# Optimization experiments

Hardware: AMD Instinct MI355X
Metric: run time of the kernel (lower is better)

The kernel has to match this reference:

```python
import math
import jax, jax.numpy as jnp
import numpy as np

X_DIM = 512
Y_DIM = 512
DS = 4
WH, WW = Y_DIM // DS, X_DIM // DS
RADIUS = 6          # search_radius
PATCH = 21          # patch_size
SIGMA = 1.0         # preprocess_sigma
DELTA = 0.2
MASK_TH = 0.05
RAIN_TH = 0.1


def _blur(x, sigma=SIGMA):
    # replicate-pad + depthwise 2D gaussian conv (matches _gaussian_blur2d)
    r = max(1, int(math.ceil(3.0 * sigma)))
    c = jnp.arange(-r, r + 1, dtype=x.dtype)
    k1 = jnp.exp(-(c * c) / (2.0 * sigma * sigma))
    k1 = k1 / jnp.sum(k1)
    k2 = jnp.outer(k1, k1)
    C = x.shape[1]
    kern = jnp.broadcast_to(k2[None, None], (C, 1, 2 * r + 1, 2 * r + 1))
    xp = jnp.pad(x, ((0, 0), (0, 0), (r, r), (r, r)), mode='edge')
    return jax.lax.conv_general_dilated(xp, kern, (1, 1), 'VALID',
                                        dimension_numbers=('NCHW', 'OIHW', 'NCHW'),
                                        feature_group_count=C)


def _resize(x, oh, ow):
    # torch bilinear, align_corners=False, no antialias
    ih, iw = x.shape[-2], x.shape[-1]
    def coords(o, i):
        s = (jnp.arange(o, dtype=jnp.float32) + 0.5) * (i / o) - 0.5
        s = jnp.maximum(s, 0.0)
        i0 = jnp.minimum(jnp.floor(s).astype(jnp.int32), i - 1)
        i1 = jnp.minimum(i0 + 1, i - 1)
        return i0, i1, s - i0.astype(jnp.float32)
    y0, y1, wy = coords(oh, ih)
    x0, x1, wx = coords(ow, iw)
    r0 = x[..., y0, :]
    r1 = x[..., y1, :]
    v00 = r0[..., x0]; v01 = r0[..., x1]
    v10 = r1[..., x0]; v11 = r1[..., x1]
    wy = wy[:, None]; wx = wx[None, :]
    return v00 * (1 - wy) * (1 - wx) + v01 * (1 - wy) * wx + v10 * wy * (1 - wx) + v11 * wy * wx


def _avg_pool(x, k):
    # avg_pool2d, stride 1, padding k//2, count_include_pad=True
    p = k // 2
    nd = x.ndim
    win = (1,) * (nd - 2) + (k, k)
    pads = ((0, 0),) * (nd - 2) + ((p, p), (p, p))
    s = jax.lax.reduce_window(x, 0.0, jax.lax.add, win, (1,) * nd, pads)
    return s / float(k * k)


def _prepare(f):
    w = jnp.log1p(jnp.maximum(f, 0.0))
    w = _resize(w, WH, WW)
    return _blur(w)


def _grid_sample_border(field, grid):
    # bilinear grid_sample, padding_mode='border', align_corners=True
    B, C, H, W = field.shape
    ix = jnp.clip((grid[..., 0] + 1.0) * 0.5 * (W - 1), 0.0, W - 1)
    iy = jnp.clip((grid[..., 1] + 1.0) * 0.5 * (H - 1), 0.0, H - 1)
    x0 = jnp.floor(ix).astype(jnp.int32); y0 = jnp.floor(iy).astype(jnp.int32)
    x1 = jnp.minimum(x0 + 1, W - 1); y1 = jnp.minimum(y0 + 1, H - 1)
    wx = (ix - x0)[..., None]; wy = (iy - y0)[..., None]
    b = jnp.arange(B)[:, None, None]
    v00 = field[b, :, y0, x0]; v01 = field[b, :, y0, x1]
    v10 = field[b, :, y1, x0]; v11 = field[b, :, y1, x1]  # each [B,H,W,C]
    out = v00 * (1 - wy) * (1 - wx) + v01 * (1 - wy) * wx + v10 * wy * (1 - wx) + v11 * wy * wx
    return jnp.transpose(out, (0, 3, 1, 2))


def setup_inputs() -> dict:
    key = jax.random.key(0)
    k1, k2, k3 = jax.random.split(key, 3)
    pred = jax.random.normal(k1, (16, 1, 512, 512), dtype=jnp.float32)
    target = jax.random.uniform(k2, (16, 1, 512, 512), dtype=jnp.float32)
    ref = jax.random.uniform(k3, (16, 1, 512, 512), dtype=jnp.float32)
    return {"pred": pred, "target": target, "ref": ref}


def reference(pred, target, ref):
    prev_w = _prepare(ref)      # [B,1,WH,WW]
    curr_w = _prepare(target)
    rain = (_resize(target, WH, WW) >= RAIN_TH).astype(jnp.float32)
    n = 2 * RADIUS + 1
    offs = jnp.arange(-RADIUS, RADIUS + 1)
    dys = jnp.repeat(offs, n)   # dy outer loop
    dxs = jnp.tile(offs, n)     # dx inner loop
    rows = jnp.arange(WH); cols = jnp.arange(WW)

    def shift_cost(dy, dx):
        # replicate-border shift of curr_w by (dy,dx), then local SSD (21x21 avg)
        sh = curr_w[:, :, jnp.clip(rows + dy, 0, WH - 1), :]
        sh = sh[:, :, :, jnp.clip(cols + dx, 0, WW - 1)]
        return _avg_pool((prev_w - sh) ** 2, PATCH)

    costs = jax.vmap(shift_cost)(dys, dxs)        # [S,B,1,WH,WW]
    best = jnp.argmin(costs, axis=0)[:, 0]        # [B,WH,WW] (first-min, matches torch)
    fx = dxs.astype(jnp.float32)[best][:, None] * rain   # [B,1,WH,WW]
    fy = dys.astype(jnp.float32)[best][:, None] * rain
    fx = _blur(fx) * rain
    fy = _blur(fy) * rain
    fx = _resize(fx, Y_DIM, X_DIM) * (X_DIM / WW)
    fy = _resize(fy, Y_DIM, X_DIM) * (Y_DIM / WH)

    yy, xx = jnp.meshgrid(jnp.linspace(-1.0, 1.0, Y_DIM),
                          jnp.linspace(-1.0, 1.0, X_DIM), indexing='ij')
    gx = xx[None] - fx[:, 0] * (2.0 / (X_DIM - 1))
    gy = yy[None] - fy[:, 0] * (2.0 / (Y_DIM - 1))
    teacher = jnp.maximum(_grid_sample_border(ref, jnp.stack([gx, gy], axis=-1)), 0.0)

    d = pred - teacher
    ad = jnp.abs(d)
    loss = jnp.where(ad < DELTA, 0.5 * d * d, DELTA * (ad - 0.5 * DELTA))  # huber
    mask = ((teacher > MASK_TH) | (target > MASK_TH)).astype(loss.dtype)
    return jnp.mean(loss * mask)
```

## Files before the change

kernel.cpp:

```cpp
#include <hip/hip_runtime.h>
#include <math.h>

#define BATCH 16
#define HR 512
#define LR 128
#define N_LR (BATCH*LR*LR)
#define N_HR (BATCH*HR*HR)
#define NSH 13
#define NSHIFT 169
#define TH 8
#define NW 8

__device__ __forceinline__ int clampi(int v, int lo, int hi){ return v<lo?lo:(v>hi?hi:v); }

__device__ __forceinline__ float gk(int t){
  const float e1 = 0.60653065971263342f;
  const float e2 = 0.13533528323661270f;
  const float e3 = 0.011108996538242306f;
  const float norm = 1.0f/(1.0f + 2.0f*(e1+e2+e3));
  int a = t < 0 ? -t : t;
  float v = (a==0) ? 1.0f : (a==1 ? e1 : (a==2 ? e2 : e3));
  return v*norm;
}

__global__ void k_downsample(const float* __restrict__ ref, const float* __restrict__ tar,
                             float* __restrict__ wref, float* __restrict__ wtar,
                             float* __restrict__ rain){
  int i = blockIdx.x*blockDim.x + threadIdx.x;
  if (i >= N_LR) return;
  int x = i & (LR-1); int y = (i >> 7) & (LR-1); int b = i >> 14;
  int base = b*HR*HR + (4*y+1)*HR + 4*x;
  float4 r1 = *(const float4*)(ref + base);
  float4 r2 = *(const float4*)(ref + base + HR);
  float4 t1 = *(const float4*)(tar + base);
  float4 t2 = *(const float4*)(tar + base + HR);
  float r00=r1.y, r01=r1.z, r10=r2.y, r11=r2.z;
  float t00=t1.y, t01=t1.z, t10=t2.y, t11=t2.z;
  wref[i] = 0.25f*(log1pf(fmaxf(r00,0.f))+log1pf(fmaxf(r01,0.f))
                 +log1pf(fmaxf(r10,0.f))+log1pf(fmaxf(r11,0.f)));
  wtar[i] = 0.25f*(log1pf(fmaxf(t00,0.f))+log1pf(fmaxf(t01,0.f))
                 +log1pf(fmaxf(t10,0.f))+log1pf(fmaxf(t11,0.f)));
  rain[i] = (0.25f*(t00+t01+t10+t11) >= 0.1f) ? 1.0f : 0.0f;
}

__global__ void k_blur2(const float* __restrict__ in0, const float* __restrict__ in1,
                        float* __restrict__ out0, float* __restrict__ out1,
                        const float* __restrict__ m0, const float* __restrict__ m1){
  const int z = blockIdx.z;
  const float* in  = z ? in1 : in0;
  float* out       = z ? out1 : out0;
  const float* msk = z ? m1 : m0;
  const int r0 = blockIdx.x * 16;
  const int bb = blockIdx.y;
  const int tid = threadIdx.x;
  const float* I = in + (bb<<14);
  __shared__ float raw[22][LR];
  __shared__ float hb[22][LR];
  for (int idx = tid; idx < 22*LR; idx += 256){
    int lr = idx >> 7, c = idx & (LR-1);
    int gr = clampi(r0 - 3 + lr, 0, LR-1);
    raw[lr][c] = I[(gr<<7) + c];
  }
  __syncthreads();
  for (int idx = tid; idx < 22*LR; idx += 256){
    int lr = idx >> 7, c = idx & (LR-1);
    float s = 0.f;
    #pragma unroll
    for (int t=-3;t<=3;++t) s += gk(t)*raw[lr][clampi(c+t,0,LR-1)];
    hb[lr][c] = s;
  }
  __syncthreads();
  for (int idx = tid; idx < 16*LR; idx += 256){
    int lr = idx >> 7, c = idx & (LR-1);
    int i = r0 + lr;
    float s = 0.f;
    #pragma unroll
    for (int t=-3;t<=3;++t) s += gk(t)*hb[clampi(i+t,0,LR-1) - (r0-3)][c];
    int gi = (bb<<14) + (i<<7) + c;
    if (msk) s *= msk[gi];
    out[gi] = s;
  }
}

template<int CTRL, int RM>
__device__ __forceinline__ float dpp_mov0(float x){
  return __int_as_float(__builtin_amdgcn_update_dpp(0, __float_as_int(x), CTRL, RM, 0xF, true));
}
__device__ __forceinline__ float prefix64(float x){
  x += dpp_mov0<0x111,0xF>(x);
  x += dpp_mov0<0x112,0xF>(x);
  x += dpp_mov0<0x114,0xF>(x);
  x += dpp_mov0<0x118,0xF>(x);
  x += dpp_mov0<0x142,0xA>(x);
  x += dpp_mov0<0x143,0xC>(x);
  return x;
}
__device__ __forceinline__ float bperm(int addr4, float v){
  return __int_as_float(__builtin_amdgcn_ds_bpermute(addr4, __float_as_int(v)));
}

struct TapCtx { int ia0, ib0, ia1, ib1; bool la0hi, lb0ok, lb1hi, selA, selB; };

__device__ __forceinline__ void horiz_update(const TapCtx& tc, float v0, float v1, int s,
                                             unsigned long long& k0ref, unsigned long long& k1ref){
  float pf0 = prefix64(v0);
  float pf1 = prefix64(v1);
  float T0 = __int_as_float(__builtin_amdgcn_readlane(__float_as_int(pf0), 63));
  float va = tc.selA ? pf0 : pf1;
  float vb = tc.selB ? pf0 : pf1;
  float a0 = bperm(tc.ia0, va) + (tc.la0hi ? T0 : 0.f);
  float b0 = tc.lb0ok ? bperm(tc.ib0, pf0) : 0.f;
  float a1 = bperm(tc.ia1, pf1) + T0;
  float b1 = bperm(tc.ib1, vb) + (tc.lb1hi ? T0 : 0.f);
  float c0 = fmaxf((a0 - b0) * (1.0f/441.0f), 0.f);
  float c1 = fmaxf((a1 - b1) * (1.0f/441.0f), 0.f);
  unsigned long long k0 = ((unsigned long long)__float_as_uint(c0) << 32) | (unsigned)s;
  unsigned long long k1 = ((unsigned long long)__float_as_uint(c1) << 32) | (unsigned)s;
  if (k0 < k0ref) k0ref = k0;
  if (k1 < k1ref) k1ref = k1;
}

__global__ void __launch_bounds__(512, 2)
k_cost_flow(const float* __restrict__ prev, const float* __restrict__ curr,
            const float* __restrict__ rain,
            float* __restrict__ fx, float* __restrict__ fy){
  const int r0 = blockIdx.x * TH;
  const int bb = blockIdx.y;
  const int tid = threadIdx.x;
  const int w = tid >> 6, lane = tid & 63;
  const float* P = prev + (bb<<14);
  const float* C = curr + (bb<<14);

  __shared__ float currT[40][LR];
  __shared__ unsigned long long mg[4][TH*LR];

  for (int idx = tid; idx < 40*LR; idx += 512){
    int lr = idx >> 7, c = idx & (LR-1);
    int gr = clampi(r0 - 16 + lr, 0, LR-1);
    currT[lr][c] = C[(gr<<7) + c];
  }

  float p0[28], p1[28];
  #pragma unroll
  for (int wr = 0; wr < 28; ++wr){
    int gr = r0 - 10 + wr;
    if (gr >= 0 && gr < LR){ p0[wr] = P[(gr<<7) + lane]; p1[wr] = P[(gr<<7) + lane + 64]; }
    else                   { p0[wr] = 0.f; p1[wr] = 0.f; }
  }
  __syncthreads();

  unsigned long long bk0[TH], bk1[TH];
  #pragma unroll
  for (int io = 0; io < TH; ++io){ bk0[io] = ~0ULL; bk1[io] = ~0ULL; }

  TapCtx tc;
  tc.ia0 = ((lane + 10) & 63) << 2;
  tc.ib0 = ((lane - 11) & 63) << 2;
  tc.ia1 = (min(lane + 10, 63)) << 2;
  tc.ib1 = ((lane + 53) & 63) << 2;
  tc.la0hi = (lane >= 54);
  tc.lb0ok = (lane >= 11);
  tc.lb1hi = (lane >= 11);
  tc.selA  = (lane >= 10);
  tc.selB  = (lane >= 53);

  const int t_lo = (NSHIFT * w) / NW;
  const int t_hi = (NSHIFT * (w+1)) / NW;

  int t = t_lo;
  while (t < t_hi){
    const int dxi  = t / NSH;
    const int dyi0 = t - dxi*NSH;
    const int ndy  = min(NSH - dyi0, t_hi - t);
    const int dx   = dxi - 6;
    const int c0   = clampi(lane + dx, 0, LR-1);
    const int c1   = clampi(lane + 64 + dx, 0, LR-1);
    float q0[28], q1[28];
    #pragma unroll
    for (int wr = 0; wr < 28; ++wr){
      q0[wr] = currT[wr + dyi0][c0];
      q1[wr] = currT[wr + dyi0][c1];
    }
    int s = dyi0*NSH + dxi;
    for (int rep = 0; rep < ndy; ++rep){
      float v0 = 0.f, v1 = 0.f;
      #pragma unroll
      for (int wr = 0; wr <= 20; ++wr){
        if (r0 - 10 + wr >= 0 && r0 - 10 + wr < LR){
          float d0 = p0[wr] - q0[wr];
          float d1 = p1[wr] - q1[wr];
          v0 = fmaf(d0, d0, v0);
          v1 = fmaf(d1, d1, v1);
        }
      }
      horiz_update(tc, v0, v1, s, bk0[0], bk1[0]);
      #pragma unroll
      for (int io = 1; io < TH; ++io){
        {
          const int wrA = io + 20;
          if (r0 - 10 + wrA < LR){
            float d0 = p0[wrA] - q0[wrA];
            float d1 = p1[wrA] - q1[wrA];
            v0 = fmaf(d0, d0, v0);
            v1 = fmaf(d1, d1, v1);
          }
          const int wrS = io - 1;
          if (r0 - 10 + wrS >= 0){
            float d0 = p0[wrS] - q0[wrS];
            float d1 = p1[wrS] - q1[wrS];
            v0 = fmaf(-d0, d0, v0);
            v1 = fmaf(-d1, d1, v1);
          }
        }
        horiz_update(tc, v0, v1, s, bk0[io], bk1[io]);
      }
      if (rep < ndy - 1){
        #pragma unroll
        for (int wr = 0; wr < 27; ++wr){ q0[wr] = q0[wr+1]; q1[wr] = q1[wr+1]; }
        q0[27] = currT[dyi0 + rep + 28][c0];
        q1[27] = currT[dyi0 + rep + 28][c1];
      }
      s += NSH;
    }
    t += ndy;
  }

  __syncthreads();
  const int g = w & 3;
  if (w < 4){
    #pragma unroll
    for (int io = 0; io < TH; ++io){
      mg[g][io*LR + lane]      = bk0[io];
      mg[g][io*LR + lane + 64] = bk1[io];
    }
  }
  __syncthreads();
  if (w >= 4){
    #pragma unroll
    for (int io = 0; io < TH; ++io){
      unsigned long long m0 = mg[g][io*LR + lane];
      unsigned long long m1 = mg[g][io*LR + lane + 64];
      mg[g][io*LR + lane]      = (bk0[io] < m0) ? bk0[io] : m0;
      mg[g][io*LR + lane + 64] = (bk1[io] < m1) ? bk1[io] : m1;
    }
  }
  __syncthreads();
  for (int p = tid; p < TH*LR; p += 512){
    unsigned long long k  = mg[0][p];
    unsigned long long k1 = mg[1][p]; if (k1 < k) k = k1;
    unsigned long long k2 = mg[2][p]; if (k2 < k) k = k2;
    unsigned long long k3 = mg[3][p]; if (k3 < k) k = k3;
    int s = (int)(k & 0xffffffffULL);
    int io = p >> 7, jj = p & (LR-1);
    int gi = (bb<<14) + ((r0+io)<<7) + jj;
    float r = rain[gi];
    fx[gi] = (float)(s % NSH - 6) * r;
    fy[gi] = (float)(s / NSH - 6) * r;
  }
}

__global__ void __launch_bounds__(256)
k_loss(const float* __restrict__ pred, const float* __restrict__ tar,
       const float* __restrict__ ref, const float* __restrict__ fxb,
       const float* __restrict__ fyb, float* __restrict__ out){
  const int t0 = blockIdx.x*256 + threadIdx.x;
  float acc = 0.f;
  #pragma unroll
  for (int it = 0; it < 2; ++it){
    const int gq  = t0 + it*524288;
    const int b   = gq >> 16;
    const int rem = gq & 65535;
    const int y   = rem >> 7;
    const int m   = rem & 127;
    const int n = y >> 2, ky = y & 3;
    int y0; float wy;
    if (ky < 2){ y0 = max(n-1, 0); wy = (n >= 1) ? (ky == 0 ? 0.625f : 0.875f) : 0.f; }
    else       { y0 = n;           wy = (ky == 2) ? 0.125f : 0.375f; }
    const int y1 = min(y0+1, LR-1);
    const int lb = b << 14;
    const float* FxR0 = fxb + lb + (y0<<7);
    const float* FxR1 = fxb + lb + (y1<<7);
    const float* FyR0 = fyb + lb + (y0<<7);
    const float* FyR1 = fyb + lb + (y1<<7);
    const int cA = max(m-1, 0), cB = m, cC = min(m+1, LR-1);
    float xA0 = FxR0[cA], xB0 = FxR0[cB], xC0 = FxR0[cC];
    float xA1 = FxR1[cA], xB1 = FxR1[cB], xC1 = FxR1[cC];
    float yA0 = FyR0[cA], yB0 = FyR0[cB], yC0 = FyR0[cC];
    float yA1 = FyR1[cA], yB1 = FyR1[cB], yC1 = FyR1[cC];
    const bool mh = (m >= 1);
    const int hb = (b<<18) + (y<<9) + (m<<2);
    float4 pd = *(const float4*)(pred + hb);
    float4 td = *(const float4*)(tar + hb);
    const float* R = ref + (b<<18);
    const float wy1 = 1.f - wy;
    #pragma unroll
    for (int k = 0; k < 4; ++k){
      float wx;
      float lo0, hi0, lo1, hi1, flo0, fhi0, flo1, fhi1;
      if (k < 2){
        wx = mh ? (k == 0 ? 0.625f : 0.875f) : 0.f;
        lo0 = mh ? xA0 : xB0;  hi0 = mh ? xB0 : xC0;
        lo1 = mh ? xA1 : xB1;  hi1 = mh ? xB1 : xC1;
        flo0 = mh ? yA0 : yB0; fhi0 = mh ? yB0 : yC0;
        flo1 = mh ? yA1 : yB1; fhi1 = mh ? yB1 : yC1;
      } else {
        wx = (k == 2) ? 0.125f : 0.375f;
        lo0 = xB0;  hi0 = xC0;  lo1 = xB1;  hi1 = xC1;
        flo0 = yB0; fhi0 = yC0; flo1 = yB1; fhi1 = yC1;
      }
      const float w00 = wy1*(1.f-wx), w01 = wy1*wx, w10 = wy*(1.f-wx), w11 = wy*wx;
      const float fxv = 4.f*(w00*lo0 + w01*hi0 + w10*lo1 + w11*hi1);
      const float fyv = 4.f*(w00*flo0 + w01*fhi0 + w10*flo1 + w11*fhi1);
      const int x = (m<<2) + k;
      float ix = fminf(fmaxf((float)x - fxv, 0.f), (float)(HR-1));
      float iy = fminf(fmaxf((float)y - fyv, 0.f), (float)(HR-1));
      int gx0 = (int)ix; int gx1 = min(gx0+1, HR-1); float gwx = ix - (float)gx0;
      int gy0 = (int)iy; int gy1 = min(gy0+1, HR-1); float gwy = iy - (float)gy0;
      float v00 = R[(gy0<<9)+gx0], v01 = R[(gy0<<9)+gx1];
      float v10 = R[(gy1<<9)+gx0], v11 = R[(gy1<<9)+gx1];
      float tt = v00*(1.f-gwy)*(1.f-gwx) + v01*(1.f-gwy)*gwx
               + v10*gwy*(1.f-gwx)       + v11*gwy*gwx;
      float teacher = fmaxf(tt, 0.f);
      float pk = ((const float*)&pd)[k];
      float tk = ((const float*)&td)[k];
      float d  = pk - teacher;
      float ad = fabsf(d);
      float l  = ad < 0.2f ? 0.5f*d*d : 0.2f*(ad - 0.1f);
      float mm = (teacher > 0.05f || tk > 0.05f) ? 1.f : 0.f;
      acc += l*mm;
    }
  }
  acc *= (1.0f/(float)N_HR);
  #pragma unroll
  for (int o = 32; o > 0; o >>= 1) acc += __shfl_down(acc, o, 64);
  __shared__ float wsum[4];
  int lane = threadIdx.x & 63, wv = threadIdx.x >> 6;
  if (lane == 0) wsum[wv] = acc;
  __syncthreads();
  if (threadIdx.x == 0) atomicAdd(out, wsum[0]+wsum[1]+wsum[2]+wsum[3]);
}

extern "C" void kernel_launch(void* const* d_in, const int* in_sizes, int n_in,
                              void* d_out, int out_size, void* d_ws, size_t ws_size,
                              hipStream_t stream){
  const float* pred = (const float*)d_in[0];
  const float* tar  = (const float*)d_in[1];
  const float* ref  = (const float*)d_in[2];
  float* out = (float*)d_out;
  float* w = (float*)d_ws;
  float* prevW = w + 0*N_LR;
  float* currW = w + 1*N_LR;
  float* rain  = w + 2*N_LR;
  float* fxb   = w + 3*N_LR;
  float* fyb   = w + 4*N_LR;
  float* dsA   = w + 5*N_LR;
  float* dsB   = w + 6*N_LR;

  hipMemsetAsync(d_out, 0, sizeof(float), stream);

  const int tb = 256, nb = (N_LR + tb - 1)/tb;
  k_downsample<<<nb, tb, 0, stream>>>(ref, tar, dsA, dsB, rain);
  k_blur2<<<dim3(8, BATCH, 2), tb, 0, stream>>>(dsA, dsB, prevW, currW, nullptr, nullptr);
  k_cost_flow<<<dim3(LR/TH, BATCH), 512, 0, stream>>>(prevW, currW, rain, dsA, dsB);
  k_blur2<<<dim3(8, BATCH, 2), tb, 0, stream>>>(dsA, dsB, fxb, fyb, rain, rain);
  k_loss<<<2048, tb, 0, stream>>>(pred, tar, ref, fxb, fyb, out);
}
```

Before: 191.3 us.

## Read shifted curr rows directly from padded LDS and specialize interior blocks

The shared curr tile is padded to 144 columns with pre-clamped horizontal borders, which removes per-shift column clamping. The register sliding window over dy is replaced by a simple per-shift loop that reads the shifted rows straight from LDS, with the shift order flipped so dx varies fastest. A template specialization drops the row-bounds predicates for interior row blocks. The horizontal tap logic now folds the T0 offset into pf1 before the permutes, which saves a few adds. The trade is many more LDS reads per shift in exchange for fewer registers and simpler control flow.

```diff
diff --git a/kernel.cpp b/kernel.cpp
--- a/kernel.cpp
+++ b/kernel.cpp
@@ -10,6 +10,8 @@
 #define NSHIFT 169
 #define TH 8
 #define NW 8
+#define CPAD 144
+#define CROWS 40
 
 __device__ __forceinline__ int clampi(int v, int lo, int hi){ return v<lo?lo:(v>hi?hi:v); }
 
@@ -99,25 +101,67 @@
   return __int_as_float(__builtin_amdgcn_ds_bpermute(addr4, __float_as_int(v)));
 }
 
-struct TapCtx { int ia0, ib0, ia1, ib1; bool la0hi, lb0ok, lb1hi, selA, selB; };
+struct TapCtx { int ia0, ib0, ia1, ib1; bool lb0ok, selA, selB; };
 
 __device__ __forceinline__ void horiz_update(const TapCtx& tc, float v0, float v1, int s,
                                              unsigned long long& k0ref, unsigned long long& k1ref){
   float pf0 = prefix64(v0);
   float pf1 = prefix64(v1);
   float T0 = __int_as_float(__builtin_amdgcn_readlane(__float_as_int(pf0), 63));
-  float va = tc.selA ? pf0 : pf1;
-  float vb = tc.selB ? pf0 : pf1;
-  float a0 = bperm(tc.ia0, va) + (tc.la0hi ? T0 : 0.f);
+  float pg1 = pf1 + T0;
+  float va = tc.selA ? pf0 : pg1;
+  float vb = tc.selB ? pf0 : pg1;
+  float a0 = bperm(tc.ia0, va);
   float b0 = tc.lb0ok ? bperm(tc.ib0, pf0) : 0.f;
-  float a1 = bperm(tc.ia1, pf1) + T0;
-  float b1 = bperm(tc.ib1, vb) + (tc.lb1hi ? T0 : 0.f);
+  float a1 = bperm(tc.ia1, pg1);
+  float b1 = bperm(tc.ib1, vb);
   float c0 = fmaxf((a0 - b0) * (1.0f/441.0f), 0.f);
   float c1 = fmaxf((a1 - b1) * (1.0f/441.0f), 0.f);
   unsigned long long k0 = ((unsigned long long)__float_as_uint(c0) << 32) | (unsigned)s;
   unsigned long long k1 = ((unsigned long long)__float_as_uint(c1) << 32) | (unsigned)s;
   if (k0 < k0ref) k0ref = k0;
   if (k1 < k1ref) k1ref = k1;
+}
+
+template<bool EDGE>
+__device__ __forceinline__ void cost_loop(int r0, int lane, int t_lo, int t_hi,
+    const float (*cT)[CPAD], const float* p0, const float* p1, const TapCtx& tc,
+    unsigned long long* bk0, unsigned long long* bk1){
+  #pragma unroll 1
+  for (int t = t_lo; t < t_hi; ++t){
+    const int dyi = t / NSH;
+    const int dxi = t - dyi*NSH;
+    const int pc = lane + dxi;
+    float v0 = 0.f, v1 = 0.f;
+    #pragma unroll
+    for (int wr = 0; wr <= 20; ++wr){
+      if (!EDGE || ((r0 - 10 + wr) >= 0 && (r0 - 10 + wr) < LR)){
+        float d0 = p0[wr] - cT[dyi + wr][pc];
+        float d1 = p1[wr] - cT[dyi + wr][pc + 64];
+        v0 = fmaf(d0, d0, v0);
+        v1 = fmaf(d1, d1, v1);
+      }
+    }
+    horiz_update(tc, v0, v1, t, bk0[0], bk1[0]);
+    #pragma unroll
+    for (int io = 1; io < TH; ++io){
+      const int wrA = io + 20;
+      if (!EDGE || ((r0 - 10 + wrA) < LR)){
+        float d0 = p0[wrA] - cT[dyi + wrA][pc];
+        float d1 = p1[wrA] - cT[dyi + wrA][pc + 64];
+        v0 = fmaf(d0, d0, v0);
+        v1 = fmaf(d1, d1, v1);
+      }
+      const int wrS = io - 1;
+      if (!EDGE || ((r0 - 10 + wrS) >= 0)){
+        float d0 = p0[wrS] - cT[dyi + wrS][pc];
+        float d1 = p1[wrS] - cT[dyi + wrS][pc + 64];
+        v0 = fmaf(-d0, d0, v0);
+        v1 = fmaf(-d1, d1, v1);
+      }
+      horiz_update(tc, v0, v1, t, bk0[io], bk1[io]);
+    }
+  }
 }
 
 __global__ void __launch_bounds__(512, 2)
@@ -131,13 +175,14 @@
   const float* P = prev + (bb<<14);
   const float* C = curr + (bb<<14);
 
-  __shared__ float currT[40][LR];
+  __shared__ float currT[CROWS][CPAD];
   __shared__ unsigned long long mg[4][TH*LR];
 
-  for (int idx = tid; idx < 40*LR; idx += 512){
-    int lr = idx >> 7, c = idx & (LR-1);
+  for (int idx = tid; idx < CROWS*CPAD; idx += 512){
+    int lr = idx / CPAD, j = idx - lr*CPAD;
     int gr = clampi(r0 - 16 + lr, 0, LR-1);
-    currT[lr][c] = C[(gr<<7) + c];
+    int gc = clampi(j - 6, 0, LR-1);
+    currT[lr][j] = C[(gr<<7) + gc];
   }
 
   float p0[28], p1[28];
@@ -158,72 +203,16 @@
   tc.ib0 = ((lane - 11) & 63) << 2;
   tc.ia1 = (min(lane + 10, 63)) << 2;
   tc.ib1 = ((lane + 53) & 63) << 2;
-  tc.la0hi = (lane >= 54);
   tc.lb0ok = (lane >= 11);
-  tc.lb1hi = (lane >= 11);
   tc.selA  = (lane >= 10);
   tc.selB  = (lane >= 53);
 
   const int t_lo = (NSHIFT * w) / NW;
   const int t_hi = (NSHIFT * (w+1)) / NW;
 
-  int t = t_lo;
-  while (t < t_hi){
-    const int dxi  = t / NSH;
-    const int dyi0 = t - dxi*NSH;
-    const int ndy  = min(NSH - dyi0, t_hi - t);
-    const int dx   = dxi - 6;
-    const int c0   = clampi(lane + dx, 0, LR-1);
-    const int c1   = clampi(lane + 64 + dx, 0, LR-1);
-    float q0[28], q1[28];
-    #pragma unroll
-    for (int wr = 0; wr < 28; ++wr){
-      q0[wr] = currT[wr + dyi0][c0];
-      q1[wr] = currT[wr + dyi0][c1];
-    }
-    int s = dyi0*NSH + dxi;
-    for (int rep = 0; rep < ndy; ++rep){
-      float v0 = 0.f, v1 = 0.f;
-      #pragma unroll
-      for (int wr = 0; wr <= 20; ++wr){
-        if (r0 - 10 + wr >= 0 && r0 - 10 + wr < LR){
-          float d0 = p0[wr] - q0[wr];
-          float d1 = p1[wr] - q1[wr];
-          v0 = fmaf(d0, d0, v0);
-          v1 = fmaf(d1, d1, v1);
-        }
-      }
-      horiz_update(tc, v0, v1, s, bk0[0], bk1[0]);
-      #pragma unroll
-      for (int io = 1; io < TH; ++io){
-        {
-          const int wrA = io + 20;
-          if (r0 - 10 + wrA < LR){
-            float d0 = p0[wrA] - q0[wrA];
-            float d1 = p1[wrA] - q1[wrA];
-            v0 = fmaf(d0, d0, v0);
-            v1 = fmaf(d1, d1, v1);
-          }
-          const int wrS = io - 1;
-          if (r0 - 10 + wrS >= 0){
-            float d0 = p0[wrS] - q0[wrS];
-            float d1 = p1[wrS] - q1[wrS];
-            v0 = fmaf(-d0, d0, v0);
-            v1 = fmaf(-d1, d1, v1);
-          }
-        }
-        horiz_update(tc, v0, v1, s, bk0[io], bk1[io]);
-      }
-      if (rep < ndy - 1){
-        #pragma unroll
-        for (int wr = 0; wr < 27; ++wr){ q0[wr] = q0[wr+1]; q1[wr] = q1[wr+1]; }
-        q0[27] = currT[dyi0 + rep + 28][c0];
-        q1[27] = currT[dyi0 + rep + 28][c1];
-      }
-      s += NSH;
-    }
-    t += ndy;
-  }
+  const bool interior = (r0 >= 10) && (r0 + TH + 9 < LR);
+  if (interior) cost_loop<false>(r0, lane, t_lo, t_hi, currT, p0, p1, tc, bk0, bk1);
+  else          cost_loop<true >(r0, lane, t_lo, t_hi, currT, p0, p1, tc, bk0, bk1);
 
   __syncthreads();
   const int g = w & 3;
```

Result: slower. 206.6 us (+8.0%).

## Split shift search across two blocks per tile and merge argmin in blur

Applied to the files above, without the earlier changes.

The cost/flow kernel now launches twice as many blocks, each covering half of the 169 shifts (85 and 84). Each block writes its packed cost|shift keys to workspace, and the flow blur kernel takes the min of the two halves, decodes dx/dy and applies the rain mask while loading its tile. The block-level reduction now uses LDS atomicMin instead of a staged multi-sync merge, and the horizontal prefix update folds the T0 offset into pf1 before the permutes. This raises grid parallelism on a small 256-block launch at the cost of extra 64-bit key traffic and one more workspace region.

```diff
diff --git a/kernel.cpp b/kernel.cpp
--- a/kernel.cpp
+++ b/kernel.cpp
@@ -45,21 +45,33 @@
 
 __global__ void k_blur2(const float* __restrict__ in0, const float* __restrict__ in1,
                         float* __restrict__ out0, float* __restrict__ out1,
-                        const float* __restrict__ m0, const float* __restrict__ m1){
+                        const float* __restrict__ m0, const float* __restrict__ m1,
+                        const unsigned long long* __restrict__ cA,
+                        const unsigned long long* __restrict__ cB){
   const int z = blockIdx.z;
-  const float* in  = z ? in1 : in0;
   float* out       = z ? out1 : out0;
   const float* msk = z ? m1 : m0;
   const int r0 = blockIdx.x * 16;
   const int bb = blockIdx.y;
   const int tid = threadIdx.x;
-  const float* I = in + (bb<<14);
   __shared__ float raw[22][LR];
   __shared__ float hb[22][LR];
   for (int idx = tid; idx < 22*LR; idx += 256){
     int lr = idx >> 7, c = idx & (LR-1);
     int gr = clampi(r0 - 3 + lr, 0, LR-1);
-    raw[lr][c] = I[(gr<<7) + c];
+    int gi = (bb<<14) + (gr<<7) + c;
+    float v;
+    if (cA){
+      unsigned long long kk0 = cA[gi], kk1 = cB[gi];
+      unsigned long long kk = (kk1 < kk0) ? kk1 : kk0;
+      int sv = (int)(kk & 0xffffffffULL);
+      int dv = z ? (sv / NSH - 6) : (sv % NSH - 6);
+      v = (float)dv * msk[gi];
+    } else {
+      const float* in = z ? in1 : in0;
+      v = in[gi];
+    }
+    raw[lr][c] = v;
   }
   __syncthreads();
   for (int idx = tid; idx < 22*LR; idx += 256){
@@ -99,19 +111,20 @@
   return __int_as_float(__builtin_amdgcn_ds_bpermute(addr4, __float_as_int(v)));
 }
 
-struct TapCtx { int ia0, ib0, ia1, ib1; bool la0hi, lb0ok, lb1hi, selA, selB; };
+struct TapCtx { int ia0, ib0, ia1, ib1; bool lb0ok, selA, selB; };
 
 __device__ __forceinline__ void horiz_update(const TapCtx& tc, float v0, float v1, int s,
                                              unsigned long long& k0ref, unsigned long long& k1ref){
   float pf0 = prefix64(v0);
   float pf1 = prefix64(v1);
   float T0 = __int_as_float(__builtin_amdgcn_readlane(__float_as_int(pf0), 63));
-  float va = tc.selA ? pf0 : pf1;
-  float vb = tc.selB ? pf0 : pf1;
-  float a0 = bperm(tc.ia0, va) + (tc.la0hi ? T0 : 0.f);
+  float pg1 = pf1 + T0;
+  float va = tc.selA ? pf0 : pg1;
+  float vb = tc.selB ? pf0 : pg1;
+  float a0 = bperm(tc.ia0, va);
   float b0 = tc.lb0ok ? bperm(tc.ib0, pf0) : 0.f;
-  float a1 = bperm(tc.ia1, pf1) + T0;
-  float b1 = bperm(tc.ib1, vb) + (tc.lb1hi ? T0 : 0.f);
+  float a1 = bperm(tc.ia1, pg1);
+  float b1 = bperm(tc.ib1, vb);
   float c0 = fmaxf((a0 - b0) * (1.0f/441.0f), 0.f);
   float c1 = fmaxf((a1 - b1) * (1.0f/441.0f), 0.f);
   unsigned long long k0 = ((unsigned long long)__float_as_uint(c0) << 32) | (unsigned)s;
@@ -122,23 +135,24 @@
 
 __global__ void __launch_bounds__(512, 2)
 k_cost_flow(const float* __restrict__ prev, const float* __restrict__ curr,
-            const float* __restrict__ rain,
-            float* __restrict__ fx, float* __restrict__ fy){
+            unsigned long long* __restrict__ c0out, unsigned long long* __restrict__ c1out){
   const int r0 = blockIdx.x * TH;
   const int bb = blockIdx.y;
+  const int z  = blockIdx.z;
   const int tid = threadIdx.x;
   const int w = tid >> 6, lane = tid & 63;
   const float* P = prev + (bb<<14);
   const float* C = curr + (bb<<14);
 
   __shared__ float currT[40][LR];
-  __shared__ unsigned long long mg[4][TH*LR];
+  __shared__ unsigned long long mgA[TH*LR];
 
   for (int idx = tid; idx < 40*LR; idx += 512){
     int lr = idx >> 7, c = idx & (LR-1);
     int gr = clampi(r0 - 16 + lr, 0, LR-1);
     currT[lr][c] = C[(gr<<7) + c];
   }
+  for (int p = tid; p < TH*LR; p += 512) mgA[p] = ~0ULL;
 
   float p0[28], p1[28];
   #pragma unroll
@@ -158,14 +172,14 @@
   tc.ib0 = ((lane - 11) & 63) << 2;
   tc.ia1 = (min(lane + 10, 63)) << 2;
   tc.ib1 = ((lane + 53) & 63) << 2;
-  tc.la0hi = (lane >= 54);
   tc.lb0ok = (lane >= 11);
-  tc.lb1hi = (lane >= 11);
   tc.selA  = (lane >= 10);
   tc.selB  = (lane >= 53);
 
-  const int t_lo = (NSHIFT * w) / NW;
-  const int t_hi = (NSHIFT * (w+1)) / NW;
+  const int base = z ? 85 : 0;
+  const int cnt  = z ? 84 : 85;
+  const int t_lo = base + (cnt * w) / NW;
+  const int t_hi = base + (cnt * (w+1)) / NW;
 
   int t = t_lo;
   while (t < t_hi){
@@ -225,37 +239,15 @@
     t += ndy;
   }
 
-  __syncthreads();
-  const int g = w & 3;
-  if (w < 4){
-    #pragma unroll
-    for (int io = 0; io < TH; ++io){
-      mg[g][io*LR + lane]      = bk0[io];
-      mg[g][io*LR + lane + 64] = bk1[io];
-    }
-  }
-  __syncthreads();
-  if (w >= 4){
-    #pragma unroll
-    for (int io = 0; io < TH; ++io){
-      unsigned long long m0 = mg[g][io*LR + lane];
-      unsigned long long m1 = mg[g][io*LR + lane + 64];
-      mg[g][io*LR + lane]      = (bk0[io] < m0) ? bk0[io] : m0;
-      mg[g][io*LR + lane + 64] = (bk1[io] < m1) ? bk1[io] : m1;
-    }
-  }
-  __syncthreads();
+  #pragma unroll
+  for (int io = 0; io < TH; ++io){
+    atomicMin(&mgA[io*LR + lane],      bk0[io]);
+    atomicMin(&mgA[io*LR + lane + 64], bk1[io]);
+  }
+  __syncthreads();
+  unsigned long long* cz = z ? c1out : c0out;
   for (int p = tid; p < TH*LR; p += 512){
-    unsigned long long k  = mg[0][p];
-    unsigned long long k1 = mg[1][p]; if (k1 < k) k = k1;
-    unsigned long long k2 = mg[2][p]; if (k2 < k) k = k2;
-    unsigned long long k3 = mg[3][p]; if (k3 < k) k = k3;
-    int s = (int)(k & 0xffffffffULL);
-    int io = p >> 7, jj = p & (LR-1);
-    int gi = (bb<<14) + ((r0+io)<<7) + jj;
-    float r = rain[gi];
-    fx[gi] = (float)(s % NSH - 6) * r;
-    fy[gi] = (float)(s / NSH - 6) * r;
+    cz[(bb<<14) + (r0<<7) + p] = mgA[p];
   }
 }
 
@@ -355,13 +347,17 @@
   float* fyb   = w + 4*N_LR;
   float* dsA   = w + 5*N_LR;
   float* dsB   = w + 6*N_LR;
+  unsigned long long* cKa = (unsigned long long*)(w + 5*N_LR);
+  unsigned long long* cKb = (unsigned long long*)(w + 7*N_LR);
 
   hipMemsetAsync(d_out, 0, sizeof(float), stream);
 
   const int tb = 256, nb = (N_LR + tb - 1)/tb;
   k_downsample<<<nb, tb, 0, stream>>>(ref, tar, dsA, dsB, rain);
-  k_blur2<<<dim3(8, BATCH, 2), tb, 0, stream>>>(dsA, dsB, prevW, currW, nullptr, nullptr);
-  k_cost_flow<<<dim3(LR/TH, BATCH), 512, 0, stream>>>(prevW, currW, rain, dsA, dsB);
-  k_blur2<<<dim3(8, BATCH, 2), tb, 0, stream>>>(dsA, dsB, fxb, fyb, rain, rain);
+  k_blur2<<<dim3(8, BATCH, 2), tb, 0, stream>>>(dsA, dsB, prevW, currW,
+                                                nullptr, nullptr, nullptr, nullptr);
+  k_cost_flow<<<dim3(LR/TH, BATCH, 2), 512, 0, stream>>>(prevW, currW, cKa, cKb);
+  k_blur2<<<dim3(8, BATCH, 2), tb, 0, stream>>>(nullptr, nullptr, fxb, fyb,
+                                                rain, rain, cKa, cKb);
   k_loss<<<2048, tb, 0, stream>>>(pred, tar, ref, fxb, fyb, out);
 }
```

Result: no change. 194.6 us (+1.7%).

## Double waves per cost block, merge argmins via shared atomicMin, fold prefix offset

Applied to the files above, without the earlier changes.

Each cost-flow block now runs 16 wavefronts instead of 8. The 169 shifts are therefore split across more waves, with launch bounds changed to 1024 threads and 1 block per CU. The staged four-slot shared-memory min reduction is replaced by 64-bit atomicMin into a single shared array, which is initialised at kernel start. The horizontal prefix fix-up is simplified by adding the wave total to the second half's prefix once, which drops several selects and adds. The risk is register pressure under the new launch bounds (large p/q register arrays) and atomic contention on shared memory.

```diff
diff --git a/kernel.cpp b/kernel.cpp
--- a/kernel.cpp
+++ b/kernel.cpp
@@ -9,7 +9,8 @@
 #define NSH 13
 #define NSHIFT 169
 #define TH 8
-#define NW 8
+#define NW 16
+#define NTHR (NW*64)
 
 __device__ __forceinline__ int clampi(int v, int lo, int hi){ return v<lo?lo:(v>hi?hi:v); }
 
@@ -99,19 +100,20 @@
   return __int_as_float(__builtin_amdgcn_ds_bpermute(addr4, __float_as_int(v)));
 }
 
-struct TapCtx { int ia0, ib0, ia1, ib1; bool la0hi, lb0ok, lb1hi, selA, selB; };
+struct TapCtx { int ia0, ib0, ia1, ib1; bool lb0ok, selA, selB; };
 
 __device__ __forceinline__ void horiz_update(const TapCtx& tc, float v0, float v1, int s,
                                              unsigned long long& k0ref, unsigned long long& k1ref){
   float pf0 = prefix64(v0);
   float pf1 = prefix64(v1);
   float T0 = __int_as_float(__builtin_amdgcn_readlane(__float_as_int(pf0), 63));
-  float va = tc.selA ? pf0 : pf1;
-  float vb = tc.selB ? pf0 : pf1;
-  float a0 = bperm(tc.ia0, va) + (tc.la0hi ? T0 : 0.f);
+  float pg1 = pf1 + T0;
+  float va = tc.selA ? pf0 : pg1;
+  float vb = tc.selB ? pf0 : pg1;
+  float a0 = bperm(tc.ia0, va);
   float b0 = tc.lb0ok ? bperm(tc.ib0, pf0) : 0.f;
-  float a1 = bperm(tc.ia1, pf1) + T0;
-  float b1 = bperm(tc.ib1, vb) + (tc.lb1hi ? T0 : 0.f);
+  float a1 = bperm(tc.ia1, pg1);
+  float b1 = bperm(tc.ib1, vb);
   float c0 = fmaxf((a0 - b0) * (1.0f/441.0f), 0.f);
   float c1 = fmaxf((a1 - b1) * (1.0f/441.0f), 0.f);
   unsigned long long k0 = ((unsigned long long)__float_as_uint(c0) << 32) | (unsigned)s;
@@ -120,7 +122,7 @@
   if (k1 < k1ref) k1ref = k1;
 }
 
-__global__ void __launch_bounds__(512, 2)
+__global__ void __launch_bounds__(NTHR, 1)
 k_cost_flow(const float* __restrict__ prev, const float* __restrict__ curr,
             const float* __restrict__ rain,
             float* __restrict__ fx, float* __restrict__ fy){
@@ -132,13 +134,14 @@
   const float* C = curr + (bb<<14);
 
   __shared__ float currT[40][LR];
-  __shared__ unsigned long long mg[4][TH*LR];
-
-  for (int idx = tid; idx < 40*LR; idx += 512){
+  __shared__ unsigned long long mgA[TH*LR];
+
+  for (int idx = tid; idx < 40*LR; idx += NTHR){
     int lr = idx >> 7, c = idx & (LR-1);
     int gr = clampi(r0 - 16 + lr, 0, LR-1);
     currT[lr][c] = C[(gr<<7) + c];
   }
+  for (int p = tid; p < TH*LR; p += NTHR) mgA[p] = ~0ULL;
 
   float p0[28], p1[28];
   #pragma unroll
@@ -158,9 +161,7 @@
   tc.ib0 = ((lane - 11) & 63) << 2;
   tc.ia1 = (min(lane + 10, 63)) << 2;
   tc.ib1 = ((lane + 53) & 63) << 2;
-  tc.la0hi = (lane >= 54);
   tc.lb0ok = (lane >= 11);
-  tc.lb1hi = (lane >= 11);
   tc.selA  = (lane >= 10);
   tc.selB  = (lane >= 53);
 
@@ -225,31 +226,14 @@
     t += ndy;
   }
 
-  __syncthreads();
-  const int g = w & 3;
-  if (w < 4){
-    #pragma unroll
-    for (int io = 0; io < TH; ++io){
-      mg[g][io*LR + lane]      = bk0[io];
-      mg[g][io*LR + lane + 64] = bk1[io];
-    }
-  }
-  __syncthreads();
-  if (w >= 4){
-    #pragma unroll
-    for (int io = 0; io < TH; ++io){
-      unsigned long long m0 = mg[g][io*LR + lane];
-      unsigned long long m1 = mg[g][io*LR + lane + 64];
-      mg[g][io*LR + lane]      = (bk0[io] < m0) ? bk0[io] : m0;
-      mg[g][io*LR + lane + 64] = (bk1[io] < m1) ? bk1[io] : m1;
-    }
-  }
-  __syncthreads();
-  for (int p = tid; p < TH*LR; p += 512){
-    unsigned long long k  = mg[0][p];
-    unsigned long long k1 = mg[1][p]; if (k1 < k) k = k1;
-    unsigned long long k2 = mg[2][p]; if (k2 < k) k = k2;
-    unsigned long long k3 = mg[3][p]; if (k3 < k) k = k3;
+  #pragma unroll
+  for (int io = 0; io < TH; ++io){
+    atomicMin(&mgA[io*LR + lane],      bk0[io]);
+    atomicMin(&mgA[io*LR + lane + 64], bk1[io]);
+  }
+  __syncthreads();
+  for (int p = tid; p < TH*LR; p += NTHR){
+    unsigned long long k = mgA[p];
     int s = (int)(k & 0xffffffffULL);
     int io = p >> 7, jj = p & (LR-1);
     int gi = (bb<<14) + ((r0+io)<<7) + jj;
@@ -361,7 +345,7 @@
   const int tb = 256, nb = (N_LR + tb - 1)/tb;
   k_downsample<<<nb, tb, 0, stream>>>(ref, tar, dsA, dsB, rain);
   k_blur2<<<dim3(8, BATCH, 2), tb, 0, stream>>>(dsA, dsB, prevW, currW, nullptr, nullptr);
-  k_cost_flow<<<dim3(LR/TH, BATCH), 512, 0, stream>>>(prevW, currW, rain, dsA, dsB);
+  k_cost_flow<<<dim3(LR/TH, BATCH), NTHR, 0, stream>>>(prevW, currW, rain, dsA, dsB);
   k_blur2<<<dim3(8, BATCH, 2), tb, 0, stream>>>(dsA, dsB, fxb, fyb, rain, rain);
   k_loss<<<2048, tb, 0, stream>>>(pred, tar, ref, fxb, fyb, out);
 }
```

New measurement: 479.5 us. +150.6%, slower.
